# Optimization experiments

Measured on AMD Instinct MI355X. Metric: run time of the kernel, lower is better.

Reference implementation:

```python
import jax, jax.numpy as jnp
import numpy as np

TAU_S = 5.0

def _psp(inputs, tau_s):
    # inputs: [..., T]; leaky integrator syn[t] = syn[t-1]*(1-1/tau) + inputs[t]
    decay = 1.0 - 1.0 / tau_s
    x = jnp.moveaxis(inputs, -1, 0)  # [T, ...]
    syn0 = jnp.zeros(x.shape[1:], dtype=x.dtype)
    def step(syn, inp):
        syn = syn * decay + inp
        return syn, syn / tau_s
    _, syns = jax.lax.scan(step, syn0, x)  # [T, ...]
    return jnp.moveaxis(syns, 0, -1)

def setup_inputs() -> dict:
    key = jax.random.key(0)
    k1, k2 = jax.random.split(key)
    outputs = jax.random.normal(k1, (128, 2048, 100), dtype=jnp.float32)
    target = jax.random.uniform(k2, (128, 2048, 100), dtype=jnp.float32)
    return {"outputs": outputs, "target": target}

def reference(outputs, target):
    target_psp = _psp(target, TAU_S)
    delta = outputs - target_psp
    return 0.5 * jnp.sum(delta ** 2)
```

## Files before the change

kernel.cpp:

```cpp
#include <hip/hip_runtime.h>


constexpr int T_LEN = 100;
constexpr int NF4   = T_LEN / 4;

typedef __attribute__((ext_vector_type(4))) float f32x4;

__global__ __launch_bounds__(256, 1) void spike_loss_main(
    const float* __restrict__ outs, const float* __restrict__ tgt,
    float* __restrict__ block_sums, int nrows)
{
    int row = blockIdx.x * blockDim.x + threadIdx.x;
    float acc = 0.0f;
    if (row < nrows) {
        const f32x4* tp = reinterpret_cast<const f32x4*>(tgt)  + (size_t)row * NF4;
        const f32x4* op = reinterpret_cast<const f32x4*>(outs) + (size_t)row * NF4;
        const float decay   = 0.8f;
        const float inv_tau = 0.2f;

        f32x4 tv[NF4], ov[NF4];
        #pragma unroll
        for (int i = 0; i < NF4; ++i) {
            tv[i] = tp[i];
            ov[i] = op[i];
        }
        __builtin_amdgcn_sched_barrier(0);

        float syn = 0.0f;
        #pragma unroll
        for (int i = 0; i < NF4; ++i) {
            float d;
            syn = fmaf(syn, decay, tv[i].x); d = fmaf(syn, -inv_tau, ov[i].x); acc = fmaf(d, d, acc);
            syn = fmaf(syn, decay, tv[i].y); d = fmaf(syn, -inv_tau, ov[i].y); acc = fmaf(d, d, acc);
            syn = fmaf(syn, decay, tv[i].z); d = fmaf(syn, -inv_tau, ov[i].z); acc = fmaf(d, d, acc);
            syn = fmaf(syn, decay, tv[i].w); d = fmaf(syn, -inv_tau, ov[i].w); acc = fmaf(d, d, acc);
        }
    }
    #pragma unroll
    for (int off = 32; off > 0; off >>= 1) acc += __shfl_down(acc, off, 64);
    __shared__ float wsum[4];
    int lane = threadIdx.x & 63;
    int wid  = threadIdx.x >> 6;
    if (lane == 0) wsum[wid] = acc;
    __syncthreads();
    if (threadIdx.x == 0) {
        block_sums[blockIdx.x] = wsum[0] + wsum[1] + wsum[2] + wsum[3];
    }
}

__global__ __launch_bounds__(256) void spike_loss_reduce(
    const float* __restrict__ block_sums, float* __restrict__ out, int n)
{
    float acc = 0.0f;
    for (int i = threadIdx.x; i < n; i += 256) acc += block_sums[i];
    #pragma unroll
    for (int off = 32; off > 0; off >>= 1) acc += __shfl_down(acc, off, 64);
    __shared__ float wsum[4];
    int lane = threadIdx.x & 63;
    int wid  = threadIdx.x >> 6;
    if (lane == 0) wsum[wid] = acc;
    __syncthreads();
    if (threadIdx.x == 0) {
        out[0] = 0.5f * (wsum[0] + wsum[1] + wsum[2] + wsum[3]);
    }
}

extern "C" void kernel_launch(void* const* d_in, const int* in_sizes, int n_in,
                              void* d_out, int out_size, void* d_ws, size_t ws_size,
                              hipStream_t stream) {
    const float* outs = (const float*)d_in[0];
    const float* tgt  = (const float*)d_in[1];
    float* out   = (float*)d_out;
    float* bsums = (float*)d_ws;

    int nrows  = in_sizes[0] / T_LEN;
    int blocks = (nrows + 255) / 256;

    spike_loss_main<<<blocks, 256, 0, stream>>>(outs, tgt, bsums, nrows);
    spike_loss_reduce<<<1, 256, 0, stream>>>(bsums, out, blocks);
}
```

Baseline: 41.66 us.

## Split each row's scan across four threads with algebraic carry correction

Each row of 100 timesteps is now handled by four threads, each running the leaky-integrator scan on its own segment from zero state. Each thread keeps the sum of squared errors plus a decay-weighted sum of errors. The missing carry-in state is then rebuilt from neighbouring lanes' final states using shuffles, and folded into the loss with a closed-form quadratic expansion using constexpr decay-power sums. This gives four times as many threads and a shorter serial dependency chain, so more memory latency can be hidden, with launch bounds raised for higher occupancy. In exchange it adds extra FMAs per element and some rounding differences from the algebraic correction.

```diff
diff --git a/kernel.cpp b/kernel.cpp
--- a/kernel.cpp
+++ b/kernel.cpp
@@ -1,47 +1,75 @@
 #include <hip/hip_runtime.h>
 
 
-constexpr int T_LEN = 100;
-constexpr int NF4   = T_LEN / 4;
+constexpr int NF4 = 25;
 
 typedef __attribute__((ext_vector_type(4))) float f32x4;
 
-__global__ __launch_bounds__(256, 1) void spike_loss_main(
+constexpr double DECAY_D = 0.8;
+constexpr float pw(double b, int n) {
+    double r = 1.0; for (int i = 0; i < n; ++i) r *= b; return (float)r;
+}
+constexpr float csum(int L) {
+    double c = 0.0, w = 0.16;
+    for (int t = 0; t < L; ++t) { c += w * w; w *= DECAY_D; }
+    return (float)c;
+}
+
+__global__ __launch_bounds__(256, 4) void spike_loss_main(
     const float* __restrict__ outs, const float* __restrict__ tgt,
-    float* __restrict__ block_sums, int nrows)
+    float* __restrict__ block_sums, int nthreads)
 {
-    int row = blockIdx.x * blockDim.x + threadIdx.x;
-    float acc = 0.0f;
-    if (row < nrows) {
-        const f32x4* tp = reinterpret_cast<const f32x4*>(tgt)  + (size_t)row * NF4;
-        const f32x4* op = reinterpret_cast<const f32x4*>(outs) + (size_t)row * NF4;
-        const float decay   = 0.8f;
-        const float inv_tau = 0.2f;
+    int tid = blockIdx.x * blockDim.x + threadIdx.x;
+    float contrib = 0.0f;
+    float syn = 0.0f;
+    float A = 0.0f, B = 0.0f;
+    int seg = tid & 3;
+    if (tid < nthreads) {
+        int row = tid >> 2;
+        int off = (seg == 0) ? 0 : (7 + (seg - 1) * 6);
+        int nf4 = (seg == 0) ? 7 : 6;
+        const f32x4* tp = reinterpret_cast<const f32x4*>(tgt)  + (size_t)row * NF4 + off;
+        const f32x4* op = reinterpret_cast<const f32x4*>(outs) + (size_t)row * NF4 + off;
 
-        f32x4 tv[NF4], ov[NF4];
+        f32x4 tv[7], ov[7];
         #pragma unroll
-        for (int i = 0; i < NF4; ++i) {
-            tv[i] = tp[i];
-            ov[i] = op[i];
+        for (int i = 0; i < 7; ++i) {
+            if (i < nf4) { tv[i] = tp[i]; ov[i] = op[i]; }
         }
         __builtin_amdgcn_sched_barrier(0);
 
-        float syn = 0.0f;
+        const float decay = 0.8f, inv_tau = 0.2f;
+        float w = 0.16f;
         #pragma unroll
-        for (int i = 0; i < NF4; ++i) {
-            float d;
-            syn = fmaf(syn, decay, tv[i].x); d = fmaf(syn, -inv_tau, ov[i].x); acc = fmaf(d, d, acc);
-            syn = fmaf(syn, decay, tv[i].y); d = fmaf(syn, -inv_tau, ov[i].y); acc = fmaf(d, d, acc);
-            syn = fmaf(syn, decay, tv[i].z); d = fmaf(syn, -inv_tau, ov[i].z); acc = fmaf(d, d, acc);
-            syn = fmaf(syn, decay, tv[i].w); d = fmaf(syn, -inv_tau, ov[i].w); acc = fmaf(d, d, acc);
+        for (int i = 0; i < 7; ++i) {
+            if (i < nf4) {
+                float d;
+                syn = fmaf(syn, decay, tv[i].x); d = fmaf(syn, -inv_tau, ov[i].x); A = fmaf(d, d, A); B = fmaf(d, w, B); w *= decay;
+                syn = fmaf(syn, decay, tv[i].y); d = fmaf(syn, -inv_tau, ov[i].y); A = fmaf(d, d, A); B = fmaf(d, w, B); w *= decay;
+                syn = fmaf(syn, decay, tv[i].z); d = fmaf(syn, -inv_tau, ov[i].z); A = fmaf(d, d, A); B = fmaf(d, w, B); w *= decay;
+                syn = fmaf(syn, decay, tv[i].w); d = fmaf(syn, -inv_tau, ov[i].w); A = fmaf(d, d, A); B = fmaf(d, w, B); w *= decay;
+            }
         }
     }
+    float l0 = __shfl(syn, 0, 4);
+    float l1 = __shfl(syn, 1, 4);
+    float l2 = __shfl(syn, 2, 4);
+    constexpr float K24 = pw(DECAY_D, 24);
+    float s = 0.0f;
+    if      (seg == 1) s = l0;
+    else if (seg == 2) s = fmaf(l0, K24, l1);
+    else if (seg == 3) s = fmaf(fmaf(l0, K24, l1), K24, l2);
+    constexpr float C28 = csum(28);
+    constexpr float C24 = csum(24);
+    float C = (seg == 0) ? C28 : C24;
+    contrib = fmaf(s * s, C, fmaf(-2.0f * s, B, A));
+
     #pragma unroll
-    for (int off = 32; off > 0; off >>= 1) acc += __shfl_down(acc, off, 64);
+    for (int offr = 32; offr > 0; offr >>= 1) contrib += __shfl_down(contrib, offr, 64);
     __shared__ float wsum[4];
     int lane = threadIdx.x & 63;
     int wid  = threadIdx.x >> 6;
-    if (lane == 0) wsum[wid] = acc;
+    if (lane == 0) wsum[wid] = contrib;
     __syncthreads();
     if (threadIdx.x == 0) {
         block_sums[blockIdx.x] = wsum[0] + wsum[1] + wsum[2] + wsum[3];
@@ -73,9 +101,10 @@
     float* out   = (float*)d_out;
     float* bsums = (float*)d_ws;
 
-    int nrows  = in_sizes[0] / T_LEN;
-    int blocks = (nrows + 255) / 256;
+    int nrows    = in_sizes[0] / 100;
+    int nthreads = nrows * 4;
+    int blocks   = (nthreads + 255) / 256;
 
-    spike_loss_main<<<blocks, 256, 0, stream>>>(outs, tgt, bsums, nrows);
+    spike_loss_main<<<blocks, 256, 0, stream>>>(outs, tgt, bsums, nthreads);
     spike_loss_reduce<<<1, 256, 0, stream>>>(bsums, out, blocks);
 }
```

After: 39.89 us. 1.04x faster.
